# Kernel tuning notes

Measured on AMD Instinct MI355X. Metric: run time of the kernel, lower is better.

The kernel has to match this reference:

```python
import jax, jax.numpy as jnp
import numpy as np

DIM = 768
HEADS = 12
HEAD_DIM = DIM // HEADS
B, N = 8, 512
LN_EPS = 1e-5


def setup_inputs() -> dict:
    key = jax.random.key(0)
    ks = jax.random.split(key, 6)
    x = jax.random.normal(ks[0], (B, N, DIM), dtype=jnp.float32)
    qkv_w = jax.random.normal(ks[1], (3 * DIM, DIM), dtype=jnp.float32) * (DIM ** -0.5)
    ln_w = jnp.ones((HEADS, N, N), dtype=jnp.float32)
    ln_b = jnp.zeros((HEADS, N, N), dtype=jnp.float32)
    proj_w = jax.random.normal(ks[2], (DIM, DIM), dtype=jnp.float32) * (DIM ** -0.5)
    proj_b = jnp.zeros((DIM,), dtype=jnp.float32)
    return {"x": x, "qkv_w": qkv_w, "ln_w": ln_w, "ln_b": ln_b,
            "proj_w": proj_w, "proj_b": proj_b}


def _grassmannian(t):
    # project each head vector onto the unit sphere (L2 normalize over head_dim)
    nrm = jnp.linalg.norm(t, axis=-1, keepdims=True)
    return t / nrm


def reference(x, qkv_w, ln_w, ln_b, proj_w, proj_b):
    b, n, c = x.shape
    qkv = (x @ qkv_w.T).reshape(b, n, 3, HEADS, HEAD_DIM)
    qkv = jnp.transpose(qkv, (2, 0, 3, 1, 4))  # (3, B, H, N, d)
    q, k, v = qkv[0], qkv[1], qkv[2]
    q = _grassmannian(q)
    k = _grassmannian(k)
    # ||outer(q_n, k_m)||_2^2 over head_dim == sum_d q_d^2 k_d^2 = (q^2) @ (k^2)^T
    attn = jnp.einsum('bhnd,bhmd->bhnm', q * q, k * k)  # (B, H, N, N)
    # LayerNorm over normalized_shape=(H, N, N), i.e. per batch element
    mean = jnp.mean(attn, axis=(1, 2, 3), keepdims=True)
    var = jnp.var(attn, axis=(1, 2, 3), keepdims=True)
    attn = (attn - mean) * jax.lax.rsqrt(var + LN_EPS) * ln_w + ln_b
    out = jnp.einsum('bhnm,bhmd->bhnd', attn, v)  # (B, H, N, d)
    out = jnp.transpose(out, (0, 2, 1, 3)).reshape(b, n, c)
    out = out @ proj_w.T + proj_b
    return out, attn
```

## Files before the change

### kernel.cpp

```cpp
#include <hip/hip_runtime.h>

typedef __attribute__((ext_vector_type(8))) short bf16x8;
typedef __attribute__((ext_vector_type(4))) float f32x4;

#define HEADS 12
#define NN 512
#define BB 8
#define DIM 768
#define LDK 72
#define LDV 136
#define OUT0_ELEMS ((size_t)BB*NN*DIM)

__device__ __forceinline__ ushort f2bf(float f) {
  union { float f; uint u; } v; v.f = f;
  uint r = v.u + 0x7fffu + ((v.u >> 16) & 1u);
  return (ushort)(r >> 16);
}

__global__ __launch_bounds__(256) void cvt_kernel(const float* __restrict__ in,
                                                  ushort* __restrict__ out, int n8) {
  int i = blockIdx.x * 256 + threadIdx.x;
  if (i >= n8) return;
  float4 a = ((const float4*)in)[i*2], b = ((const float4*)in)[i*2+1];
  uint4 o;
  o.x = f2bf(a.x) | ((uint)f2bf(a.y) << 16);
  o.y = f2bf(a.z) | ((uint)f2bf(a.w) << 16);
  o.z = f2bf(b.x) | ((uint)f2bf(b.y) << 16);
  o.w = f2bf(b.z) | ((uint)f2bf(b.w) << 16);
  ((uint4*)out)[i] = o;
}

__global__ __launch_bounds__(256) void qkv_gemm(
    const ushort* __restrict__ xb, const ushort* __restrict__ wb,
    ushort* __restrict__ q2b, ushort* __restrict__ k2b, ushort* __restrict__ vt)
{
  __shared__ ushort As[128 * LDK];
  __shared__ ushort Bs[128 * LDK];
  const int t = threadIdx.x, l = t & 63, w = t >> 6;
  const int bx = blockIdx.x, by = blockIdx.y;
  const int rowbase = by * 128, colbase = bx * 128;
  const int wr = w >> 1, wc = w & 1, lr = l & 15, lg = l >> 4;
  f32x4 acc[4][4] = {};

  for (int kc = 0; kc < DIM; kc += 64) {
    #pragma unroll
    for (int i = 0; i < 4; ++i) {
      int c = t + 256 * i;
      int r = c >> 3, k16 = c & 7;
      *(uint4*)(As + r * LDK + k16 * 8) =
          *(const uint4*)(xb + (size_t)(rowbase + r) * DIM + kc + k16 * 8);
      *(uint4*)(Bs + r * LDK + k16 * 8) =
          *(const uint4*)(wb + (size_t)(colbase + r) * DIM + kc + k16 * 8);
    }
    __syncthreads();
    #pragma unroll
    for (int ks = 0; ks < 2; ++ks) {
      bf16x8 af[4], bg[4];
      #pragma unroll
      for (int i = 0; i < 4; ++i)
        af[i] = *(const bf16x8*)(As + (wr*64 + i*16 + lr) * LDK + ks*32 + lg*8);
      #pragma unroll
      for (int j = 0; j < 4; ++j)
        bg[j] = *(const bf16x8*)(Bs + (wc*64 + j*16 + lr) * LDK + ks*32 + lg*8);
      #pragma unroll
      for (int i = 0; i < 4; ++i)
        #pragma unroll
        for (int j = 0; j < 4; ++j)
          acc[i][j] = __builtin_amdgcn_mfma_f32_16x16x32_bf16(af[i], bg[j], acc[i][j], 0, 0, 0);
    }
    __syncthreads();
  }

  const int gcol = colbase + wc * 64;
  const int sel = gcol / DIM;
  const int h = (gcol % DIM) / 64;
  if (sel < 2) {
    ushort* dst = (sel == 0) ? q2b : k2b;
    #pragma unroll
    for (int i = 0; i < 4; ++i) {
      #pragma unroll
      for (int r = 0; r < 4; ++r) {
        float vj[4]; float s = 0.f;
        #pragma unroll
        for (int j = 0; j < 4; ++j) { vj[j] = acc[i][j][r]; s += vj[j] * vj[j]; }
        #pragma unroll
        for (int off = 1; off < 16; off <<= 1) s += __shfl_xor(s, off);
        float inv = 1.0f / s;
        int row = rowbase + wr*64 + i*16 + lg*4 + r;
        int b = row >> 9, n = row & 511;
        ushort* o = dst + (((size_t)(b * HEADS + h) * NN + n) << 6);
        #pragma unroll
        for (int j = 0; j < 4; ++j) o[j*16 + lr] = f2bf(vj[j] * vj[j] * inv);
      }
    }
  } else {
    #pragma unroll
    for (int i = 0; i < 4; ++i) {
      int row0 = rowbase + wr*64 + i*16 + lg*4;
      int b = row0 >> 9, n0 = row0 & 511;
      #pragma unroll
      for (int j = 0; j < 4; ++j) {
        int d = j*16 + lr;
        ushort4 pk;
        pk.x = f2bf(acc[i][j][0]); pk.y = f2bf(acc[i][j][1]);
        pk.z = f2bf(acc[i][j][2]); pk.w = f2bf(acc[i][j][3]);
        *(ushort4*)(vt + (((size_t)(b * HEADS + h) * 64 + d) << 9) + n0) = pk;
      }
    }
  }
}

__global__ __launch_bounds__(256) void stats_kernel(
    const ushort* __restrict__ q2b, const ushort* __restrict__ k2b,
    double* __restrict__ hsum)
{
  __shared__ ushort Qs[256 * LDK];
  __shared__ ushort Ks[128 * LDK];
  __shared__ float red[8];
  const int t = threadIdx.x, l = t & 63, w = t >> 6;
  const int rt = blockIdx.x, h = blockIdx.y, b = blockIdx.z;
  const size_t bh = (size_t)(b * HEADS + h);
  const int rowbase = rt * 256;
  const int lr = l & 15, lg = l >> 4;
  #pragma unroll
  for (int i = 0; i < 8; ++i) {
    int c = t + 256 * i;
    int r = c >> 3, k16 = c & 7;
    *(uint4*)(Qs + r * LDK + k16 * 8) =
        *(const uint4*)(q2b + (bh << 15) + ((size_t)(rowbase + r) << 6) + k16 * 8);
  }
  float s1 = 0.f, s2 = 0.f;
  for (int ct = 0; ct < 4; ++ct) {
    #pragma unroll
    for (int i = 0; i < 4; ++i) {
      int c = t + 256 * i;
      int r = c >> 3, k16 = c & 7;
      *(uint4*)(Ks + r * LDK + k16 * 8) =
          *(const uint4*)(k2b + (bh << 15) + ((size_t)(ct*128 + r) << 6) + k16 * 8);
    }
    __syncthreads();
    bf16x8 af[4][2];
    #pragma unroll
    for (int i = 0; i < 4; ++i)
      #pragma unroll
      for (int ks = 0; ks < 2; ++ks)
        af[i][ks] = *(const bf16x8*)(Qs + (w*64 + i*16 + lr) * LDK + ks*32 + lg*8);
    #pragma unroll
    for (int j = 0; j < 8; ++j) {
      bf16x8 b0 = *(const bf16x8*)(Ks + (j*16 + lr) * LDK + lg*8);
      bf16x8 b1 = *(const bf16x8*)(Ks + (j*16 + lr) * LDK + 32 + lg*8);
      #pragma unroll
      for (int i = 0; i < 4; ++i) {
        f32x4 a = {};
        a = __builtin_amdgcn_mfma_f32_16x16x32_bf16(af[i][0], b0, a, 0, 0, 0);
        a = __builtin_amdgcn_mfma_f32_16x16x32_bf16(af[i][1], b1, a, 0, 0, 0);
        #pragma unroll
        for (int r = 0; r < 4; ++r) { s1 += a[r]; s2 += a[r]*a[r]; }
      }
    }
    __syncthreads();
  }
  #pragma unroll
  for (int off = 1; off < 64; off <<= 1) { s1 += __shfl_xor(s1, off); s2 += __shfl_xor(s2, off); }
  if (l == 0) { red[w] = s1; red[4 + w] = s2; }
  __syncthreads();
  if (t == 0) {
    double d1 = (double)red[0] + red[1] + red[2] + red[3];
    double d2 = (double)red[4] + red[5] + red[6] + red[7];
    atomicAdd(&hsum[b * 2], d1);
    atomicAdd(&hsum[b * 2 + 1], d2);
  }
}

__global__ __launch_bounds__(256) void norm_pv(
    const ushort* __restrict__ q2b, const ushort* __restrict__ k2b,
    const ushort* __restrict__ vt,
    const float* __restrict__ lnw, const float* __restrict__ lnb,
    const double* __restrict__ hsum,
    float* __restrict__ attn, ushort* __restrict__ obh)
{
  __shared__ ushort Qs[64 * LDK];
  __shared__ ushort Ks[128 * LDK];
  __shared__ ushort Vs[64 * LDV];
  __shared__ ushort Ps[64 * LDV];
  const int t = threadIdx.x, l = t & 63, w = t >> 6;
  const int rt = blockIdx.x, h = blockIdx.y, b = blockIdx.z;
  const size_t bh = (size_t)(b * HEADS + h);
  const int rowbase = rt * 64;
  const int lr = l & 15, lg = l >> 4;
  const double cnt = (double)HEADS * NN * NN;
  double mu = hsum[b * 2] / cnt;
  double var = hsum[b * 2 + 1] / cnt - mu * mu;
  const float mean = (float)mu;
  const float istd = (float)(1.0 / sqrt(var + 1e-5));

  #pragma unroll
  for (int i = 0; i < 2; ++i) {
    int c = t + 256 * i;
    int r = c >> 3, k16 = c & 7;
    *(uint4*)(Qs + r * LDK + k16 * 8) =
        *(const uint4*)(q2b + (bh << 15) + ((size_t)(rowbase + r) << 6) + k16 * 8);
  }
  f32x4 opv[4] = {};

  for (int ct = 0; ct < 4; ++ct) {
    #pragma unroll
    for (int i = 0; i < 4; ++i) {
      int c = t + 256 * i;
      int r = c >> 3, k16 = c & 7;
      *(uint4*)(Ks + r * LDK + k16 * 8) =
          *(const uint4*)(k2b + (bh << 15) + ((size_t)(ct*128 + r) << 6) + k16 * 8);
    }
    #pragma unroll
    for (int i = 0; i < 4; ++i) {
      int c = t + 256 * i;
      int r = c >> 4, k16 = c & 15;
      *(uint4*)(Vs + r * LDV + k16 * 8) =
          *(const uint4*)(vt + (bh << 15) + ((size_t)r << 9) + ct*128 + k16 * 8);
    }
    __syncthreads();
    #pragma unroll
    for (int i = 0; i < 4; ++i) {
      bf16x8 a0 = *(const bf16x8*)(Qs + (i*16 + lr) * LDK + lg*8);
      bf16x8 a1 = *(const bf16x8*)(Qs + (i*16 + lr) * LDK + 32 + lg*8);
      #pragma unroll
      for (int j = 0; j < 2; ++j) {
        bf16x8 b0 = *(const bf16x8*)(Ks + (w*32 + j*16 + lr) * LDK + lg*8);
        bf16x8 b1 = *(const bf16x8*)(Ks + (w*32 + j*16 + lr) * LDK + 32 + lg*8);
        f32x4 a = {};
        a = __builtin_amdgcn_mfma_f32_16x16x32_bf16(a0, b0, a, 0, 0, 0);
        a = __builtin_amdgcn_mfma_f32_16x16x32_bf16(a1, b1, a, 0, 0, 0);
        const int nl = i*16 + lg*4;
        const int ml = w*32 + j*16 + lr;
        const int n = rowbase + nl;
        const int m = ct*128 + ml;
        const float* lwp = lnw + ((size_t)h * NN + n) * NN + m;
        const float* lbp = lnb + ((size_t)h * NN + n) * NN + m;
        float* ap = attn + ((bh << 9) + n) * NN + m;
        #pragma unroll
        for (int r = 0; r < 4; ++r) {
          float v = (a[r] - mean) * istd * lwp[(size_t)r * NN] + lbp[(size_t)r * NN];
          __builtin_nontemporal_store(v, ap + (size_t)r * NN);
          Ps[(nl + r) * LDV + ml] = f2bf(v);
        }
      }
    }
    __syncthreads();
    #pragma unroll
    for (int ks = 0; ks < 4; ++ks) {
      bf16x8 ap = *(const bf16x8*)(Ps + (w*16 + lr) * LDV + ks*32 + lg*8);
      #pragma unroll
      for (int j = 0; j < 4; ++j) {
        bf16x8 bv = *(const bf16x8*)(Vs + (j*16 + lr) * LDV + ks*32 + lg*8);
        opv[j] = __builtin_amdgcn_mfma_f32_16x16x32_bf16(ap, bv, opv[j], 0, 0, 0);
      }
    }
    __syncthreads();
  }
  #pragma unroll
  for (int j = 0; j < 4; ++j) {
    int gc = h * 64 + j*16 + lr;
    #pragma unroll
    for (int r = 0; r < 4; ++r) {
      int gr = b * NN + rowbase + w*16 + lg*4 + r;
      obh[(size_t)gr * DIM + gc] = f2bf(opv[j][r]);
    }
  }
}

__global__ __launch_bounds__(256) void proj_gemm(
    const ushort* __restrict__ obh, const ushort* __restrict__ pwb,
    const float* __restrict__ pb, float* __restrict__ out)
{
  __shared__ ushort As[128 * LDK];
  __shared__ ushort Bs[128 * LDK];
  const int t = threadIdx.x, l = t & 63, w = t >> 6;
  const int bx = blockIdx.x, by = blockIdx.y;
  const int rowbase = by * 128, colbase = bx * 128;
  const int wr = w >> 1, wc = w & 1, lr = l & 15, lg = l >> 4;
  f32x4 acc[4][4] = {};
  for (int kc = 0; kc < DIM; kc += 64) {
    #pragma unroll
    for (int i = 0; i < 4; ++i) {
      int c = t + 256 * i;
      int r = c >> 3, k16 = c & 7;
      *(uint4*)(As + r * LDK + k16 * 8) =
          *(const uint4*)(obh + (size_t)(rowbase + r) * DIM + kc + k16 * 8);
      *(uint4*)(Bs + r * LDK + k16 * 8) =
          *(const uint4*)(pwb + (size_t)(colbase + r) * DIM + kc + k16 * 8);
    }
    __syncthreads();
    #pragma unroll
    for (int ks = 0; ks < 2; ++ks) {
      bf16x8 af[4], bg[4];
      #pragma unroll
      for (int i = 0; i < 4; ++i)
        af[i] = *(const bf16x8*)(As + (wr*64 + i*16 + lr) * LDK + ks*32 + lg*8);
      #pragma unroll
      for (int j = 0; j < 4; ++j)
        bg[j] = *(const bf16x8*)(Bs + (wc*64 + j*16 + lr) * LDK + ks*32 + lg*8);
      #pragma unroll
      for (int i = 0; i < 4; ++i)
        #pragma unroll
        for (int j = 0; j < 4; ++j)
          acc[i][j] = __builtin_amdgcn_mfma_f32_16x16x32_bf16(af[i], bg[j], acc[i][j], 0, 0, 0);
    }
    __syncthreads();
  }
  #pragma unroll
  for (int i = 0; i < 4; ++i) {
    #pragma unroll
    for (int r = 0; r < 4; ++r) {
      int row = rowbase + wr*64 + i*16 + lg*4 + r;
      #pragma unroll
      for (int j = 0; j < 4; ++j) {
        int col = colbase + wc*64 + j*16 + lr;
        out[(size_t)row * DIM + col] = acc[i][j][r] + pb[col];
      }
    }
  }
}

extern "C" void kernel_launch(void* const* d_in, const int* in_sizes, int n_in,
                              void* d_out, int out_size, void* d_ws, size_t ws_size,
                              hipStream_t stream) {
  const float* x      = (const float*)d_in[0];
  const float* qkv_w  = (const float*)d_in[1];
  const float* ln_w   = (const float*)d_in[2];
  const float* ln_b   = (const float*)d_in[3];
  const float* proj_w = (const float*)d_in[4];
  const float* proj_b = (const float*)d_in[5];
  float* out      = (float*)d_out;
  float* attn_out = out + OUT0_ELEMS;

  char* ws = (char*)d_ws;
  double* hsum = (double*)ws;
  ushort* wb   = (ushort*)(ws + 256);
  ushort* pwb  = wb  + (size_t)2304 * 768;
  ushort* xb   = pwb + (size_t)768 * 768;
  ushort* q2b  = xb  + (size_t)4096 * 768;
  ushort* k2b  = q2b + ((size_t)BB * HEADS * NN << 6);
  ushort* vt   = k2b + ((size_t)BB * HEADS * NN << 6);
  ushort* obh  = vt  + ((size_t)BB * HEADS * NN << 6);

  hipMemsetAsync(hsum, 0, 128, stream);
  cvt_kernel<<<dim3(864),  256, 0, stream>>>(qkv_w,  wb,  221184);
  cvt_kernel<<<dim3(288),  256, 0, stream>>>(proj_w, pwb, 73728);
  cvt_kernel<<<dim3(1536), 256, 0, stream>>>(x,      xb,  393216);
  qkv_gemm    <<<dim3(18, 32),        256, 0, stream>>>(xb, wb, q2b, k2b, vt);
  stats_kernel<<<dim3(2, HEADS, BB),  256, 0, stream>>>(q2b, k2b, hsum);
  norm_pv     <<<dim3(8, HEADS, BB),  256, 0, stream>>>(q2b, k2b, vt, ln_w, ln_b, hsum,
                                                        attn_out, obh);
  proj_gemm   <<<dim3(6, 32),         256, 0, stream>>>(obh, pwb, proj_b, out);
}
```

Baseline: 259.9 us.

## Merge conversion kernels and transpose QK^T tile for vectorized attn epilogue

Folds the three fp32-to-bf16 conversion launches into one kernel that dispatches by index range, saving two launches. In norm_pv the score MFMA swaps operands (K as A, Q as B, with Q fragments kept in registers), so each lane holds four consecutive columns. That lets the LayerNorm weight and bias loads and the attn stores become float4 accesses instead of strided scalar ones. The bf16 P tile is packed with v_cvt_pk_bf16_f32 into an XOR-swizzled shared layout to avoid bank conflicts, at the cost of more register pressure from the held Q fragments.

```diff
diff --git a/kernel.cpp b/kernel.cpp
--- a/kernel.cpp
+++ b/kernel.cpp
@@ -17,16 +17,21 @@
   return (ushort)(r >> 16);
 }
 
-__global__ __launch_bounds__(256) void cvt_kernel(const float* __restrict__ in,
-                                                  ushort* __restrict__ out, int n8) {
+__global__ __launch_bounds__(256) void cvt3_kernel(
+    const float* __restrict__ a, ushort* __restrict__ oa, int na8,
+    const float* __restrict__ b, ushort* __restrict__ ob, int nb8,
+    const float* __restrict__ c, ushort* __restrict__ oc, int nc8) {
   int i = blockIdx.x * 256 + threadIdx.x;
-  if (i >= n8) return;
-  float4 a = ((const float4*)in)[i*2], b = ((const float4*)in)[i*2+1];
+  const float* in; ushort* out;
+  if (i < na8) { in = a; out = oa; }
+  else if (i < na8 + nb8) { i -= na8; in = b; out = ob; }
+  else { i -= na8 + nb8; if (i >= nc8) return; in = c; out = oc; }
+  float4 x = ((const float4*)in)[i*2], y = ((const float4*)in)[i*2+1];
   uint4 o;
-  o.x = f2bf(a.x) | ((uint)f2bf(a.y) << 16);
-  o.y = f2bf(a.z) | ((uint)f2bf(a.w) << 16);
-  o.z = f2bf(b.x) | ((uint)f2bf(b.y) << 16);
-  o.w = f2bf(b.z) | ((uint)f2bf(b.w) << 16);
+  o.x = f2bf(x.x) | ((uint)f2bf(x.y) << 16);
+  o.y = f2bf(x.z) | ((uint)f2bf(x.w) << 16);
+  o.z = f2bf(y.x) | ((uint)f2bf(y.y) << 16);
+  o.w = f2bf(y.z) | ((uint)f2bf(y.w) << 16);
   ((uint4*)out)[i] = o;
 }
 
@@ -182,7 +187,7 @@
   __shared__ ushort Qs[64 * LDK];
   __shared__ ushort Ks[128 * LDK];
   __shared__ ushort Vs[64 * LDV];
-  __shared__ ushort Ps[64 * LDV];
+  __shared__ ushort Pb[64 * 128];
   const int t = threadIdx.x, l = t & 63, w = t >> 6;
   const int rt = blockIdx.x, h = blockIdx.y, b = blockIdx.z;
   const size_t bh = (size_t)(b * HEADS + h);
@@ -201,6 +206,14 @@
     *(uint4*)(Qs + r * LDK + k16 * 8) =
         *(const uint4*)(q2b + (bh << 15) + ((size_t)(rowbase + r) << 6) + k16 * 8);
   }
+  __syncthreads();
+  bf16x8 qf[4][2];
+  #pragma unroll
+  for (int j = 0; j < 4; ++j)
+    #pragma unroll
+    for (int ks = 0; ks < 2; ++ks)
+      qf[j][ks] = *(const bf16x8*)(Qs + (j*16 + lr) * LDK + ks*32 + lg*8);
+
   f32x4 opv[4] = {};
 
   for (int ct = 0; ct < 4; ++ct) {
@@ -220,35 +233,43 @@
     }
     __syncthreads();
     #pragma unroll
-    for (int i = 0; i < 4; ++i) {
-      bf16x8 a0 = *(const bf16x8*)(Qs + (i*16 + lr) * LDK + lg*8);
-      bf16x8 a1 = *(const bf16x8*)(Qs + (i*16 + lr) * LDK + 32 + lg*8);
-      #pragma unroll
-      for (int j = 0; j < 2; ++j) {
-        bf16x8 b0 = *(const bf16x8*)(Ks + (w*32 + j*16 + lr) * LDK + lg*8);
-        bf16x8 b1 = *(const bf16x8*)(Ks + (w*32 + j*16 + lr) * LDK + 32 + lg*8);
+    for (int i = 0; i < 2; ++i) {
+      bf16x8 a0 = *(const bf16x8*)(Ks + (w*32 + i*16 + lr) * LDK + lg*8);
+      bf16x8 a1 = *(const bf16x8*)(Ks + (w*32 + i*16 + lr) * LDK + 32 + lg*8);
+      const int mloc = w*32 + i*16 + lg*4;
+      const int m0 = ct*128 + mloc;
+      const int cch = mloc >> 3;
+      #pragma unroll
+      for (int j = 0; j < 4; ++j) {
         f32x4 a = {};
-        a = __builtin_amdgcn_mfma_f32_16x16x32_bf16(a0, b0, a, 0, 0, 0);
-        a = __builtin_amdgcn_mfma_f32_16x16x32_bf16(a1, b1, a, 0, 0, 0);
-        const int nl = i*16 + lg*4;
-        const int ml = w*32 + j*16 + lr;
-        const int n = rowbase + nl;
-        const int m = ct*128 + ml;
-        const float* lwp = lnw + ((size_t)h * NN + n) * NN + m;
-        const float* lbp = lnb + ((size_t)h * NN + n) * NN + m;
-        float* ap = attn + ((bh << 9) + n) * NN + m;
-        #pragma unroll
-        for (int r = 0; r < 4; ++r) {
-          float v = (a[r] - mean) * istd * lwp[(size_t)r * NN] + lbp[(size_t)r * NN];
-          __builtin_nontemporal_store(v, ap + (size_t)r * NN);
-          Ps[(nl + r) * LDV + ml] = f2bf(v);
-        }
+        a = __builtin_amdgcn_mfma_f32_16x16x32_bf16(a0, qf[j][0], a, 0, 0, 0);
+        a = __builtin_amdgcn_mfma_f32_16x16x32_bf16(a1, qf[j][1], a, 0, 0, 0);
+        const int n = j*16 + lr;
+        const size_t rowoff = ((size_t)h * NN + rowbase + n) * NN + m0;
+        const float4 lw4 = *(const float4*)(lnw + rowoff);
+        const float4 lb4 = *(const float4*)(lnb + rowoff);
+        f32x4 v;
+        v[0] = (a[0] - mean) * istd * lw4.x + lb4.x;
+        v[1] = (a[1] - mean) * istd * lw4.y + lb4.y;
+        v[2] = (a[2] - mean) * istd * lw4.z + lb4.z;
+        v[3] = (a[3] - mean) * istd * lw4.w + lb4.w;
+        __builtin_nontemporal_store(v,
+            (f32x4*)(attn + ((bh << 9) + rowbase + n) * NN + m0));
+        uint pk01, pk23;
+        asm("v_cvt_pk_bf16_f32 %0, %1, %2" : "=v"(pk01) : "v"(v[0]), "v"(v[1]));
+        asm("v_cvt_pk_bf16_f32 %0, %1, %2" : "=v"(pk23) : "v"(v[2]), "v"(v[3]));
+        const int pch = (cch & 8) | ((cch & 7) ^ (n & 7));
+        uint2 pk = { pk01, pk23 };
+        *(uint2*)(Pb + n*128 + pch*8 + (lg & 1)*4) = pk;
       }
     }
     __syncthreads();
     #pragma unroll
     for (int ks = 0; ks < 4; ++ks) {
-      bf16x8 ap = *(const bf16x8*)(Ps + (w*16 + lr) * LDV + ks*32 + lg*8);
+      const int cc = ks*4 + lg;
+      const int nl = w*16 + lr;
+      const int pch = (cc & 8) | ((cc & 7) ^ (nl & 7));
+      bf16x8 ap = *(const bf16x8*)(Pb + nl*128 + pch*8);
       #pragma unroll
       for (int j = 0; j < 4; ++j) {
         bf16x8 bv = *(const bf16x8*)(Vs + (j*16 + lr) * LDV + ks*32 + lg*8);
@@ -344,9 +365,9 @@
   ushort* obh  = vt  + ((size_t)BB * HEADS * NN << 6);
 
   hipMemsetAsync(hsum, 0, 128, stream);
-  cvt_kernel<<<dim3(864),  256, 0, stream>>>(qkv_w,  wb,  221184);
-  cvt_kernel<<<dim3(288),  256, 0, stream>>>(proj_w, pwb, 73728);
-  cvt_kernel<<<dim3(1536), 256, 0, stream>>>(x,      xb,  393216);
+  cvt3_kernel<<<dim3(2688), 256, 0, stream>>>(qkv_w, wb, 221184,
+                                              proj_w, pwb, 73728,
+                                              x, xb, 393216);
   qkv_gemm    <<<dim3(18, 32),        256, 0, stream>>>(xb, wb, q2b, k2b, vt);
   stats_kernel<<<dim3(2, HEADS, BB),  256, 0, stream>>>(q2b, k2b, hsum);
   norm_pv     <<<dim3(8, HEADS, BB),  256, 0, stream>>>(q2b, k2b, vt, ln_w, ln_b, hsum,
```

Measured after the change: 263.7 us. No clear change (+1.5%).
